# Performance work log

Hardware: AMD Instinct MI355X
Metric: run time of the kernel (lower is better)

Reference implementation:

```python
import jax, jax.numpy as jnp
import numpy as np


def setup_inputs() -> dict:
    key = jax.random.key(0)
    k1, k2 = jax.random.split(key)
    N, D = 8192, 1024
    x = jax.random.normal(k1, (N, D), dtype=jnp.float32)
    w = jax.random.normal(k2, (D, 1), dtype=jnp.float32)
    return {"x": x, "w": w}


def reference(x, w):
    # x: [N, D], w: [D, 1]
    N = x.shape[0]
    a = jax.nn.sigmoid(x @ w)[:, 0]          # [N], values in (0, 1)
    b = jnp.cumsum(a)                         # [N] running sum
    idx = jnp.floor(b).astype(jnp.int32)      # bin index per column
    prev = jnp.concatenate([jnp.zeros(1, jnp.int32), idx[:-1]])
    same = idx == prev                        # did we stay in the same bin?
    frac = b - idx.astype(b.dtype)            # portion falling into bin `idx`
    cols = jnp.arange(N)
    # value written at [idx, i]: a_i if same bin, else the fractional overflow
    main_val = jnp.where(same, a, frac)
    # cross-boundary remainder written at [idx-1, i]
    cross_val = jnp.where(same, 0.0, a - frac)
    cross_row = jnp.where(same, idx, idx - 1)  # dummy (add 0) when same
    trans_mat = (
        jnp.zeros((N, N), dtype=x.dtype)
        .at[idx, cols].set(main_val)
        .at[cross_row, cols].add(cross_val)
    )
    return trans_mat @ x                      # [N, D]
```

## Files before the change

kernel.cpp:

```cpp
#include <hip/hip_runtime.h>
#include <math.h>


__global__ void dot_sigmoid_kernel(const float* __restrict__ x,
                                   const float* __restrict__ w,
                                   float* __restrict__ a, int N, int D) {
  int lane = threadIdx.x & 63;
  int wave = threadIdx.x >> 6;
  int row = blockIdx.x * (blockDim.x >> 6) + wave;
  if (row >= N) return;
  const float4* xr = reinterpret_cast<const float4*>(x + (size_t)row * D);
  const float4* w4 = reinterpret_cast<const float4*>(w);
  float acc = 0.f;
  int nv = D >> 2;
  for (int j = lane; j < nv; j += 64) {
    float4 xv = xr[j];
    float4 wv = w4[j];
    acc = fmaf(xv.x, wv.x, acc);
    acc = fmaf(xv.y, wv.y, acc);
    acc = fmaf(xv.z, wv.z, acc);
    acc = fmaf(xv.w, wv.w, acc);
  }
#pragma unroll
  for (int off = 32; off > 0; off >>= 1) acc += __shfl_down(acc, off, 64);
  if (lane == 0) a[row] = 1.0f / (1.0f + expf(-acc));
}

__global__ __launch_bounds__(1024) void scan_kernel(const float* __restrict__ a,
                                                    float* __restrict__ mainv,
                                                    float* __restrict__ crossv,
                                                    int* __restrict__ idxv,
                                                    int* __restrict__ rowptr, int N) {
  __shared__ float sa[8192];
  __shared__ double wtot[16];
  __shared__ double woff[16];
  int t = threadIdx.x;
  for (int k = t; k < N; k += 1024) sa[k] = a[k];
  for (int k = t; k <= N; k += 1024) rowptr[k] = N;
  if (t == 0) rowptr[0] = 0;
  __syncthreads();

  const int per = 8;
  int base = t * per;
  double loc[8];
  double run = 0.0;
#pragma unroll
  for (int j = 0; j < 8; ++j) {
    run += (double)sa[base + j];
    loc[j] = run;
  }
  double v = run;
  int lane = t & 63;
  int wid = t >> 6;
  for (int off = 1; off < 64; off <<= 1) {
    double n = __shfl_up(v, off, 64);
    if (lane >= off) v += n;
  }
  if (lane == 63) wtot[wid] = v;
  __syncthreads();
  if (t == 0) {
    double s = 0.0;
    for (int q = 0; q < 16; ++q) { woff[q] = s; s += wtot[q]; }
  }
  __syncthreads();
  double pre = woff[wid] + (v - run);
  double prevbd = pre;
#pragma unroll
  for (int j = 0; j < 8; ++j) {
    int i = base + j;
    double bd = pre + loc[j];
    float bf = (float)bd;
    float pf = (float)prevbd;
    int k = (int)floorf(bf);
    int kp = (int)floorf(pf);
    float ai = sa[i];
    float frac = bf - (float)k;
    bool same = (k == kp);
    mainv[i] = same ? ai : frac;
    crossv[i] = same ? 0.f : (ai - frac);
    idxv[i] = k;
    if (!same) rowptr[k] = i;
    prevbd = bd;
  }
}

constexpr int R = 8;
constexpr int CAP = 1024;

__global__ __launch_bounds__(256) void out_kernel(
    const float* __restrict__ x, const float* __restrict__ mainv,
    const float* __restrict__ crossv, const int* __restrict__ idxv,
    const int* __restrict__ rowptr, float* __restrict__ out, int N, int D) {
  __shared__ float sm[CAP];
  __shared__ float sc[CAP];
  __shared__ int sk[CAP];
  int r0 = blockIdx.x * R;
  int s_begin = rowptr[r0];
  int s_endp = rowptr[r0 + R];
  int len = s_endp - s_begin;
  int total = len + (s_endp < N ? 1 : 0);
  int t = threadIdx.x;
  bool use_lds = (s_begin < N) && (total <= CAP);
  if (use_lds) {
    for (int j = t; j < total; j += 256) {
      sm[j] = mainv[s_begin + j];
      sc[j] = crossv[s_begin + j];
      sk[j] = idxv[s_begin + j];
    }
    __syncthreads();
  }
  int c = t << 2;
  float4 acc = make_float4(0.f, 0.f, 0.f, 0.f);
  int cur = r0;
  for (int j = 0; j < len; ++j) {
    int i = s_begin + j;
    float wm, wc;
    int k;
    if (use_lds) { wm = sm[j]; wc = sc[j]; k = sk[j]; }
    else         { wm = mainv[i]; wc = crossv[i]; k = idxv[i]; }
    if (k > cur) {
      while (cur < k - 1) {
        *reinterpret_cast<float4*>(out + (size_t)cur * D + c) = acc;
        acc = make_float4(0.f, 0.f, 0.f, 0.f);
        ++cur;
      }
      float4 xv = *reinterpret_cast<const float4*>(x + (size_t)i * D + c);
      acc.x = fmaf(wc, xv.x, acc.x);
      acc.y = fmaf(wc, xv.y, acc.y);
      acc.z = fmaf(wc, xv.z, acc.z);
      acc.w = fmaf(wc, xv.w, acc.w);
      *reinterpret_cast<float4*>(out + (size_t)cur * D + c) = acc;
      cur = k;
      acc.x = wm * xv.x;
      acc.y = wm * xv.y;
      acc.z = wm * xv.z;
      acc.w = wm * xv.w;
    } else if (wm >= 1e-7f) {
      float4 xv = *reinterpret_cast<const float4*>(x + (size_t)i * D + c);
      acc.x = fmaf(wm, xv.x, acc.x);
      acc.y = fmaf(wm, xv.y, acc.y);
      acc.z = fmaf(wm, xv.z, acc.z);
      acc.w = fmaf(wm, xv.w, acc.w);
    }
  }
  if (s_endp < N) {
    float wc = use_lds ? sc[len] : crossv[s_endp];
    float4 xv = *reinterpret_cast<const float4*>(x + (size_t)s_endp * D + c);
    acc.x = fmaf(wc, xv.x, acc.x);
    acc.y = fmaf(wc, xv.y, acc.y);
    acc.z = fmaf(wc, xv.z, acc.z);
    acc.w = fmaf(wc, xv.w, acc.w);
  }
  *reinterpret_cast<float4*>(out + (size_t)cur * D + c) = acc;
  float4 z = make_float4(0.f, 0.f, 0.f, 0.f);
  for (int r = cur + 1; r < r0 + R; ++r)
    *reinterpret_cast<float4*>(out + (size_t)r * D + c) = z;
}

extern "C" void kernel_launch(void* const* d_in, const int* in_sizes, int n_in,
                              void* d_out, int out_size, void* d_ws, size_t ws_size,
                              hipStream_t stream) {
  const float* x = (const float*)d_in[0];
  const float* w = (const float*)d_in[1];
  float* out = (float*)d_out;
  int D = in_sizes[1];
  int N = in_sizes[0] / D;

  float* a = (float*)d_ws;
  float* mainv = a + N;
  float* crossv = mainv + N;
  int* idxv = (int*)(crossv + N);
  int* rowptr = idxv + N;

  hipLaunchKernelGGL(dot_sigmoid_kernel, dim3(N / 4), dim3(256), 0, stream,
                     x, w, a, N, D);
  hipLaunchKernelGGL(scan_kernel, dim3(1), dim3(1024), 0, stream,
                     a, mainv, crossv, idxv, rowptr, N);
  hipLaunchKernelGGL(out_kernel, dim3(N / R), dim3(256), 0, stream,
                     x, mainv, crossv, idxv, rowptr, out, N, D);
}
```

Measured before the change: 107.4 us.

## Parallelize prefix scan across blocks using per-chunk sums from dot kernel

The single-block scan kernel is replaced by a multi-block scan. The dot-sigmoid kernel now also initializes rowptr and atomically accumulates per-256-row chunk sums in double. Each scan block then adds up the preceding chunk sums and does a local wave scan. This removes the serial one-block scan bottleneck, at the cost of an extra memset, double atomics, and larger 1024-thread blocks in the dot kernel. Summation order now depends on atomic ordering, which could shift floor boundaries slightly between runs.

```diff
diff --git a/kernel.cpp b/kernel.cpp
--- a/kernel.cpp
+++ b/kernel.cpp
@@ -2,13 +2,15 @@
 #include <math.h>
 
 
-__global__ void dot_sigmoid_kernel(const float* __restrict__ x,
-                                   const float* __restrict__ w,
-                                   float* __restrict__ a, int N, int D) {
-  int lane = threadIdx.x & 63;
-  int wave = threadIdx.x >> 6;
-  int row = blockIdx.x * (blockDim.x >> 6) + wave;
-  if (row >= N) return;
+__global__ __launch_bounds__(1024) void dot_sigmoid_kernel(
+    const float* __restrict__ x, const float* __restrict__ w,
+    float* __restrict__ a, double* __restrict__ chunksum,
+    int* __restrict__ rowptr, int N, int D) {
+  __shared__ float was[16];
+  int t = threadIdx.x;
+  int lane = t & 63;
+  int wave = t >> 6;
+  int row = blockIdx.x * 16 + wave;
   const float4* xr = reinterpret_cast<const float4*>(x + (size_t)row * D);
   const float4* w4 = reinterpret_cast<const float4*>(w);
   float acc = 0.f;
@@ -23,65 +25,60 @@
   }
 #pragma unroll
   for (int off = 32; off > 0; off >>= 1) acc += __shfl_down(acc, off, 64);
-  if (lane == 0) a[row] = 1.0f / (1.0f + expf(-acc));
+  if (lane == 0) {
+    float av = 1.0f / (1.0f + expf(-acc));
+    a[row] = av;
+    was[wave] = av;
+  }
+  int gtid = blockIdx.x * 1024 + t;
+  if (gtid <= N) rowptr[gtid] = N;
+  __syncthreads();
+  if (t == 0) {
+    double s = 0.0;
+    for (int q = 0; q < 16; ++q) s += (double)was[q];
+    atomicAdd(&chunksum[blockIdx.x >> 4], s);
+  }
 }
 
-__global__ __launch_bounds__(1024) void scan_kernel(const float* __restrict__ a,
-                                                    float* __restrict__ mainv,
-                                                    float* __restrict__ crossv,
-                                                    int* __restrict__ idxv,
-                                                    int* __restrict__ rowptr, int N) {
-  __shared__ float sa[8192];
-  __shared__ double wtot[16];
-  __shared__ double woff[16];
+__global__ __launch_bounds__(256) void scan_emit_kernel(
+    const float* __restrict__ a, const double* __restrict__ chunksum,
+    float* __restrict__ mainv, float* __restrict__ crossv,
+    int* __restrict__ idxv, int* __restrict__ rowptr, int N) {
+  __shared__ double spre_s;
+  __shared__ double wtot[4];
+  int b = blockIdx.x;
   int t = threadIdx.x;
-  for (int k = t; k < N; k += 1024) sa[k] = a[k];
-  for (int k = t; k <= N; k += 1024) rowptr[k] = N;
-  if (t == 0) rowptr[0] = 0;
-  __syncthreads();
-
-  const int per = 8;
-  int base = t * per;
-  double loc[8];
-  double run = 0.0;
-#pragma unroll
-  for (int j = 0; j < 8; ++j) {
-    run += (double)sa[base + j];
-    loc[j] = run;
-  }
-  double v = run;
+  int i = b * 256 + t;
   int lane = t & 63;
   int wid = t >> 6;
+  float ai = a[i];
+  if (t == 0) {
+    double s = 0.0;
+    for (int q = 0; q < b; ++q) s += chunksum[q];
+    spre_s = s;
+    if (b == 0) rowptr[0] = 0;
+  }
+  double v = (double)ai;
   for (int off = 1; off < 64; off <<= 1) {
     double n = __shfl_up(v, off, 64);
     if (lane >= off) v += n;
   }
   if (lane == 63) wtot[wid] = v;
   __syncthreads();
-  if (t == 0) {
-    double s = 0.0;
-    for (int q = 0; q < 16; ++q) { woff[q] = s; s += wtot[q]; }
-  }
-  __syncthreads();
-  double pre = woff[wid] + (v - run);
-  double prevbd = pre;
-#pragma unroll
-  for (int j = 0; j < 8; ++j) {
-    int i = base + j;
-    double bd = pre + loc[j];
-    float bf = (float)bd;
-    float pf = (float)prevbd;
-    int k = (int)floorf(bf);
-    int kp = (int)floorf(pf);
-    float ai = sa[i];
-    float frac = bf - (float)k;
-    bool same = (k == kp);
-    mainv[i] = same ? ai : frac;
-    crossv[i] = same ? 0.f : (ai - frac);
-    idxv[i] = k;
-    if (!same) rowptr[k] = i;
-    prevbd = bd;
-  }
+  double pre = spre_s;
+  for (int q = 0; q < wid; ++q) pre += wtot[q];
+  double bd = pre + v;
+  double prevbd = bd - (double)ai;
+  float bf = (float)bd;
+  float pf = (float)prevbd;
+  int k = (int)floorf(bf);
+  int kp = (int)floorf(pf);
+  float frac = bf - (float)k;
+  bool same = (k == kp);
+  mainv[i] = same ? ai : frac;
+  crossv[i] = same ? 0.f : (ai - frac);
+  idxv[i] = k;
+  if (!same) rowptr[k] = i;
 }
 
 constexpr int R = 8;
@@ -171,11 +168,14 @@
   float* crossv = mainv + N;
   int* idxv = (int*)(crossv + N);
   int* rowptr = idxv + N;
+  double* chunksum = (double*)(((uintptr_t)(rowptr + N + 1) + 15) & ~15ull);
 
-  hipLaunchKernelGGL(dot_sigmoid_kernel, dim3(N / 4), dim3(256), 0, stream,
-                     x, w, a, N, D);
-  hipLaunchKernelGGL(scan_kernel, dim3(1), dim3(1024), 0, stream,
-                     a, mainv, crossv, idxv, rowptr, N);
+  hipMemsetAsync(chunksum, 0, 32 * sizeof(double), stream);
+
+  hipLaunchKernelGGL(dot_sigmoid_kernel, dim3(N / 16), dim3(1024), 0, stream,
+                     x, w, a, chunksum, rowptr, N, D);
+  hipLaunchKernelGGL(scan_emit_kernel, dim3(N / 256), dim3(256), 0, stream,
+                     a, chunksum, mainv, crossv, idxv, rowptr, N);
   hipLaunchKernelGGL(out_kernel, dim3(N / R), dim3(256), 0, stream,
                      x, mainv, crossv, idxv, rowptr, out, N, D);
 }
```

Result: faster. 100.9 us (-6.0%).
